# Kernel optimization log

Measured on AMD Instinct MI355X. Metric: run time of the kernel, lower is better.

Reference implementation:

```python
import jax, jax.numpy as jnp
import numpy as np

HEADS = 4
HID = 32
IN_CH = 3
N = 50000
E = 800000


def setup_inputs() -> dict:
    key = jax.random.key(0)
    ks = jax.random.split(key, 16)
    d1 = HEADS * HID  # 128
    s = 0.1
    inp = {
        'x': jax.random.normal(ks[0], (N, IN_CH), jnp.float32),
        'edge_index': jax.random.randint(ks[1], (2, E), 0, N, jnp.int64),
        # layer 1: in=3 -> heads*hid
        'W1': jax.random.normal(ks[2], (IN_CH, d1), jnp.float32) * s,
        'as1': jax.random.normal(ks[3], (HEADS, HID), jnp.float32) * s,
        'ad1': jax.random.normal(ks[4], (HEADS, HID), jnp.float32) * s,
        'b1': jnp.zeros((d1,), jnp.float32),
        # layer 2: 128 -> 128
        'W2': jax.random.normal(ks[5], (d1, d1), jnp.float32) * s,
        'as2': jax.random.normal(ks[6], (HEADS, HID), jnp.float32) * s,
        'ad2': jax.random.normal(ks[7], (HEADS, HID), jnp.float32) * s,
        'b2': jnp.zeros((d1,), jnp.float32),
        # layer 3: 128 -> 128
        'W3': jax.random.normal(ks[8], (d1, d1), jnp.float32) * s,
        'as3': jax.random.normal(ks[9], (HEADS, HID), jnp.float32) * s,
        'ad3': jax.random.normal(ks[10], (HEADS, HID), jnp.float32) * s,
        'b3': jnp.zeros((d1,), jnp.float32),
        # classifier: 128 -> 1
        'cW': jax.random.normal(ks[11], (d1, 1), jnp.float32) * s,
        'cb': jnp.zeros((1,), jnp.float32),
    }
    return inp


def _gat_layer(x, src, dst, n, W, a_s, a_d, b):
    """PyG GATConv (concat=True, negative_slope=0.2, self-loops already added)."""
    xp = (x @ W).reshape(n, HEADS, HID)              # [N,H,C]
    al_s = jnp.einsum('nhc,hc->nh', xp, a_s)          # [N,H]
    al_d = jnp.einsum('nhc,hc->nh', xp, a_d)          # [N,H]
    e = jax.nn.leaky_relu(al_s[src] + al_d[dst], 0.2)  # [E',H]
    emax = jax.ops.segment_max(e, dst, num_segments=n)  # segment softmax over dst
    ex = jnp.exp(e - emax[dst])
    den = jax.ops.segment_sum(ex, dst, num_segments=n)
    alpha = ex / (den[dst] + 1e-16)                   # [E',H]
    msg = xp[src] * alpha[:, :, None]                 # [E',H,C]
    out = jax.ops.segment_sum(msg, dst, num_segments=n)  # [N,H,C]
    return out.reshape(n, HEADS * HID) + b


def reference(x, edge_index, W1, as1, ad1, b1, W2, as2, ad2, b2, W3, as3, ad3, b3, cW, cb):
    n = x.shape[0]
    loops = jnp.arange(n, dtype=edge_index.dtype)
    src = jnp.concatenate([edge_index[0], loops])     # add self-loops (PyG default)
    dst = jnp.concatenate([edge_index[1], loops])
    h = jax.nn.elu(_gat_layer(x, src, dst, n, W1, as1, ad1, b1))
    h = jax.nn.elu(_gat_layer(h, src, dst, n, W2, as2, ad2, b2))
    h = jax.nn.elu(_gat_layer(h, src, dst, n, W3, as3, ad3, b3))
    logits = (h @ cW + cb)[:, 0]                      # [N]
    return jax.nn.sigmoid(logits)                     # eval mode output
```

## Files before the change

kernel.cpp:

```cpp
#include <hip/hip_runtime.h>
#include <math.h>

typedef unsigned int uint_t;
typedef __attribute__((ext_vector_type(8))) short bf16x8;
typedef __attribute__((ext_vector_type(4))) float f32x4;

#define BK_SHIFT 7
#define BK_NODES 128
#define MAXBK 512
#define PART_CHUNK 4096
#define SORT_CAP 4096

__device__ __forceinline__ float lrelu(float x){ return x > 0.f ? x : 0.2f*x; }
__device__ __forceinline__ float sel4(float a, float b, float c, float d, int h){
    return h==0 ? a : (h==1 ? b : (h==2 ? c : d));
}
__device__ __forceinline__ float wsum(float v){
    #pragma unroll
    for (int m = 1; m < 64; m <<= 1) v += __shfl_xor(v, m);
    return v;
}
__device__ __forceinline__ uint_t pack_bf2(float a, float b){
    uint_t ua = __float_as_uint(a); uint_t ub = __float_as_uint(b);
    ua += 0x7FFFu + ((ua >> 16) & 1u);
    ub += 0x7FFFu + ((ub >> 16) & 1u);
    return (ua >> 16) | (ub & 0xFFFF0000u);
}
__device__ __forceinline__ float bflo(uint_t u){ return __uint_as_float(u << 16); }
__device__ __forceinline__ float bfhi(uint_t u){ return __uint_as_float(u & 0xFFFF0000u); }
__device__ __forceinline__ bf16x8 mk_bf8(uint4 u){
    bf16x8 r;
    r[0]=(short)(u.x & 0xFFFFu); r[1]=(short)(u.x >> 16);
    r[2]=(short)(u.y & 0xFFFFu); r[3]=(short)(u.y >> 16);
    r[4]=(short)(u.z & 0xFFFFu); r[5]=(short)(u.z >> 16);
    r[6]=(short)(u.w & 0xFFFFu); r[7]=(short)(u.w >> 16);
    return r;
}


__global__ __launch_bounds__(256) void bucket_count(const int* __restrict__ ei, int E, int N,
                                                    int* __restrict__ bkcnt){
    __shared__ int h[MAXBK];
    int t = threadIdx.x;
    for (int i = t; i < MAXBK; i += 256) h[i] = 0;
    __syncthreads();
    int base = blockIdx.x * PART_CHUNK;
    int cnt = E + N - base; if (cnt > PART_CHUNK) cnt = PART_CHUNK; if (cnt < 0) cnt = 0;
    for (int i = t; i < cnt; i += 256){
        int idx = base + i;
        int d = (idx < E) ? ei[E + idx] : (idx - E);
        atomicAdd(&h[d >> BK_SHIFT], 1);
    }
    __syncthreads();
    for (int i = t; i < MAXBK; i += 256) if (h[i]) atomicAdd(&bkcnt[i], h[i]);
}

__global__ __launch_bounds__(512) void bucket_scan(const int* __restrict__ bkcnt,
                                                   int* __restrict__ bkoff,
                                                   int* __restrict__ gcursor,
                                                   int NBK, int EN){
    int t = threadIdx.x;
    __shared__ int sm[MAXBK];
    sm[t] = (t < NBK) ? bkcnt[t] : 0;
    __syncthreads();
    for (int off = 1; off < MAXBK; off <<= 1){
        int u = (t >= off) ? sm[t - off] : 0;
        __syncthreads();
        sm[t] += u;
        __syncthreads();
    }
    int excl = (t == 0) ? 0 : sm[t - 1];
    if (t < NBK){ bkoff[t] = excl; gcursor[t] = excl; }
    if (t == 0) bkoff[NBK] = EN;
}

__global__ __launch_bounds__(256) void partition_kernel(
        const int* __restrict__ ei, int E, int N,
        int* __restrict__ gcursor, uint_t* __restrict__ pairbuf, int NBK){
    __shared__ int hist[MAXBK];
    __shared__ int sA[MAXBK];
    __shared__ int destadj[MAXBK];
    __shared__ int cnt2[MAXBK];
    __shared__ uint_t staged[PART_CHUNK];
    __shared__ unsigned short sbk[PART_CHUNK];
    int t = threadIdx.x;
    int base = blockIdx.x * PART_CHUNK;
    int total = E + N;
    int cnt = total - base; if (cnt > PART_CHUNK) cnt = PART_CHUNK; if (cnt < 0) cnt = 0;

    for (int i = t; i < MAXBK; i += 256){ hist[i] = 0; cnt2[i] = 0; }
    __syncthreads();
    for (int i = t; i < cnt; i += 256){
        int idx = base + i;
        int d = (idx < E) ? ei[E + idx] : (idx - E);
        atomicAdd(&hist[d >> BK_SHIFT], 1);
    }
    __syncthreads();
    sA[t] = hist[t]; sA[t + 256] = hist[t + 256];
    __syncthreads();
    for (int off = 1; off < MAXBK; off <<= 1){
        int i0 = t, i1 = t + 256;
        int a0 = sA[i0] + ((i0 >= off) ? sA[i0 - off] : 0);
        int a1 = sA[i1] + ((i1 >= off) ? sA[i1 - off] : 0);
        __syncthreads();
        sA[i0] = a0; sA[i1] = a1;
        __syncthreads();
    }
    for (int b = t; b < NBK; b += 256){
        int c = hist[b];
        int gstart = (b == 0) ? 0 : sA[b - 1];
        int rbase = c > 0 ? atomicAdd(&gcursor[b], c) : 0;
        destadj[b] = rbase - gstart;
        cnt2[b] = gstart;
    }
    __syncthreads();
    for (int i = t; i < cnt; i += 256){
        int idx = base + i;
        int d, s;
        if (idx < E){ s = ei[idx]; d = ei[E + idx]; }
        else        { s = d = idx - E; }
        int b = d >> BK_SHIFT;
        int pos = atomicAdd(&cnt2[b], 1);
        staged[pos] = (uint_t)s | ((uint_t)(d & (BK_NODES - 1)) << 25);
        sbk[pos] = (unsigned short)b;
    }
    __syncthreads();
    for (int p = t; p < cnt; p += 256){
        int b = (int)sbk[p];
        pairbuf[destadj[b] + p] = staged[p];
    }
}

__global__ __launch_bounds__(256) void bucket_sort2(
        const uint_t* __restrict__ pairbuf, const int* __restrict__ bkoff,
        int* __restrict__ indptr, int* __restrict__ srcs, int N, int NBK, int EN){
    int b = blockIdx.x;
    int beg = bkoff[b], end = bkoff[b + 1];
    int cnt = end - beg;
    int nb = b << BK_SHIFT;
    __shared__ int nh[BK_NODES];
    __shared__ int noff[BK_NODES];
    __shared__ int outb[SORT_CAP];
    int t = threadIdx.x;
    if (t < BK_NODES) nh[t] = 0;
    __syncthreads();
    for (int i = t; i < cnt; i += 256){
        uint_t pr = pairbuf[beg + i];
        atomicAdd(&nh[(int)(pr >> 25)], 1);
    }
    __syncthreads();
    if (t < BK_NODES) noff[t] = nh[t];
    __syncthreads();
    for (int off = 1; off < BK_NODES; off <<= 1){
        int u = 0;
        if (t < BK_NODES && t >= off) u = noff[t - off];
        __syncthreads();
        if (t < BK_NODES) noff[t] += u;
        __syncthreads();
    }
    if (t < BK_NODES){
        int excl = noff[t] - nh[t];
        int node = nb + t;
        if (node < N) indptr[node] = beg + excl;
        nh[t] = excl;
    }
    if (b == NBK - 1 && t == 0) indptr[N] = EN;
    __syncthreads();
    if (cnt <= SORT_CAP){
        for (int i = t; i < cnt; i += 256){
            uint_t pr = pairbuf[beg + i];
            int pos = atomicAdd(&nh[(int)(pr >> 25)], 1);
            outb[pos] = (int)(pr & 0x1FFFFFFu);
        }
        __syncthreads();
        for (int i = t; i < cnt; i += 256) srcs[beg + i] = outb[i];
    } else {
        for (int i = t; i < cnt; i += 256){
            uint_t pr = pairbuf[beg + i];
            int pos = atomicAdd(&nh[(int)(pr >> 25)], 1);
            srcs[beg + pos] = (int)(pr & 0x1FFFFFFu);
        }
    }
}

__global__ __launch_bounds__(128) void linear_al(
        const float* __restrict__ in, const float* __restrict__ W,
        const float* __restrict__ as_, const float* __restrict__ ad_,
        uint_t* __restrict__ xp16, float* __restrict__ als, float* __restrict__ ald,
        int N, int K){
    __shared__ float hs[8 * 3];
    int t = threadIdx.x;
    int base = blockIdx.x * 8;
    int rows = N - base; if (rows > 8) rows = 8;
    for (int idx = t; idx < rows * K; idx += 128){
        int r = idx / K, k = idx - r * K;
        hs[r * K + k] = in[(size_t)(base + r) * K + k];
    }
    __syncthreads();
    float acc[8] = {0.f,0.f,0.f,0.f,0.f,0.f,0.f,0.f};
    for (int k = 0; k < K; ++k){
        float w = W[k * 128 + t];
        #pragma unroll
        for (int r = 0; r < 8; ++r) acc[r] += hs[r * K + k] * w;
    }
    float asv = as_[t], adv = ad_[t];
    for (int r = 0; r < rows; ++r){
        int row = base + r;
        float v = acc[r];
        float vo = __shfl_xor(v, 1);
        if (!(t & 1)) xp16[(size_t)row * 64 + (t >> 1)] = pack_bf2(v, vo);
        float vs = v * asv, vd = v * adv;
        #pragma unroll
        for (int m = 16; m >= 1; m >>= 1){
            vs += __shfl_xor(vs, m);
            vd += __shfl_xor(vd, m);
        }
        if ((t & 31) == 0){
            int h = t >> 5;
            als[row * 4 + h] = vs;
            ald[row * 4 + h] = vd;
        }
    }
}

__global__ __launch_bounds__(256) void wpack_kernel(
        const float* __restrict__ W2, const float* __restrict__ W3,
        uint_t* __restrict__ B2, uint_t* __restrict__ B3){
    int idx = blockIdx.x * 256 + threadIdx.x;
    const float* W = (idx < 8192) ? W2 : W3;
    uint_t* Bp = (idx < 8192) ? B2 : B3;
    int i = idx & 8191;
    int u = i & 3, c = (i >> 2) & 15, kg = (i >> 6) & 3, kb = (i >> 8) & 3, cb = (i >> 10) & 7;
    int k = kb * 32 + kg * 8 + 2 * u;
    int col = cb * 16 + c;
    Bp[i] = pack_bf2(W[k * 128 + col], W[(k + 1) * 128 + col]);
}

__global__ __launch_bounds__(256) void gemm_mfma(
        const uint_t* __restrict__ h16, const uint_t* __restrict__ bpack,
        const float* __restrict__ as_, const float* __restrict__ ad_,
        uint_t* __restrict__ xp16, float* __restrict__ als, float* __restrict__ ald,
        int N){
    int w = threadIdx.x >> 6;
    int l = threadIdx.x & 63;
    int stripe = blockIdx.x * 4 + w;
    int base = stripe * 16;
    if (base >= N) return;
    int r16 = l & 15;
    int kg  = l >> 4;
    int row = base + r16;
    int rowc = row < N ? row : N - 1;

    bf16x8 afr[4];
    const uint4* hrow = (const uint4*)(h16 + (size_t)rowc * 64);
    #pragma unroll
    for (int kb = 0; kb < 4; ++kb) afr[kb] = mk_bf8(hrow[kb * 4 + kg]);

    f32x4 acc[8];
    #pragma unroll
    for (int cb = 0; cb < 8; ++cb) acc[cb] = (f32x4){0.f, 0.f, 0.f, 0.f};

    const uint4* bp = (const uint4*)bpack;
    #pragma unroll
    for (int cb = 0; cb < 8; ++cb){
        #pragma unroll
        for (int kb = 0; kb < 4; ++kb){
            bf16x8 bfr = mk_bf8(bp[((cb * 4 + kb) * 4 + kg) * 16 + r16]);
            acc[cb] = __builtin_amdgcn_mfma_f32_16x16x32_bf16(afr[kb], bfr, acc[cb], 0, 0, 0);
        }
    }

    #pragma unroll
    for (int reg = 0; reg < 4; ++reg){
        int ro = base + kg * 4 + reg;
        bool wr = (ro < N) && ((r16 & 1) == 0);
        #pragma unroll
        for (int cb = 0; cb < 8; ++cb){
            float v  = acc[cb][reg];
            float vo = __shfl_xor(v, 1);
            if (wr) xp16[(size_t)ro * 64 + cb * 8 + (r16 >> 1)] = pack_bf2(v, vo);
        }
        #pragma unroll
        for (int h = 0; h < 4; ++h){
            float a0 = as_[h * 32 + r16],      a1 = as_[h * 32 + 16 + r16];
            float g0 = ad_[h * 32 + r16],      g1 = ad_[h * 32 + 16 + r16];
            float ps = acc[2 * h][reg] * a0 + acc[2 * h + 1][reg] * a1;
            float pd = acc[2 * h][reg] * g0 + acc[2 * h + 1][reg] * g1;
            ps += __shfl_xor(ps, 1); ps += __shfl_xor(ps, 2);
            ps += __shfl_xor(ps, 4); ps += __shfl_xor(ps, 8);
            pd += __shfl_xor(pd, 1); pd += __shfl_xor(pd, 2);
            pd += __shfl_xor(pd, 4); pd += __shfl_xor(pd, 8);
            if (r16 == 0 && ro < N){
                als[(size_t)ro * 4 + h] = ps;
                ald[(size_t)ro * 4 + h] = pd;
            }
        }
    }
}

__global__ __launch_bounds__(256, 8) void gat_agg4(
        const uint_t* __restrict__ xp16, const float4* __restrict__ als,
        const float4* __restrict__ ald,
        const int* __restrict__ indptr, const int* __restrict__ srcs,
        const float* __restrict__ bias,
        uint_t* __restrict__ hout, int N, int mode,
        const float* __restrict__ cW, const float* __restrict__ cb,
        float* __restrict__ fout){
    int wid = threadIdx.x >> 6;
    int l   = threadIdx.x & 63;
    int n = blockIdx.x * 4 + wid;
    __shared__ int   ssh[4][64];
    __shared__ float esh[4][64][4];
    if (n >= N) return;

    int beg = indptr[n], end = indptr[n + 1];
    float4 ad4 = ald[n];
    int h = l >> 4;

    float d0 = 0.f, d1 = 0.f, d2 = 0.f, d3 = 0.f;
    float ax = 0.f, ay = 0.f;

    for (int cbeg = beg; cbeg < end; cbeg += 64){
        int cnt = end - cbeg; if (cnt > 64) cnt = 64;
        if (l < cnt){
            int s = srcs[cbeg + l];
            ssh[wid][l] = s;
            float4 a4 = als[s];
            float p0 = __expf(lrelu(a4.x + ad4.x));
            float p1 = __expf(lrelu(a4.y + ad4.y));
            float p2 = __expf(lrelu(a4.z + ad4.z));
            float p3 = __expf(lrelu(a4.w + ad4.w));
            *((float4*)&esh[wid][l][0]) = make_float4(p0, p1, p2, p3);
            d0 += p0; d1 += p1; d2 += p2; d3 += p3;
        }
        __builtin_amdgcn_wave_barrier();

        int j = 0;
        for (; j + 16 <= cnt; j += 16){
            int ss[16]; float ww[16]; uint_t uu[16];
            #pragma unroll
            for (int q = 0; q < 16; ++q){ ss[q] = ssh[wid][j+q]; ww[q] = esh[wid][j+q][h]; }
            #pragma unroll
            for (int q = 0; q < 16; ++q) uu[q] = xp16[(size_t)ss[q] * 64 + l];
            #pragma unroll
            for (int q = 0; q < 16; ++q){
                ax = fmaf(bflo(uu[q]), ww[q], ax);
                ay = fmaf(bfhi(uu[q]), ww[q], ay);
            }
        }
        for (; j + 8 <= cnt; j += 8){
            int ss[8]; float ww[8]; uint_t uu[8];
            #pragma unroll
            for (int q = 0; q < 8; ++q){ ss[q] = ssh[wid][j+q]; ww[q] = esh[wid][j+q][h]; }
            #pragma unroll
            for (int q = 0; q < 8; ++q) uu[q] = xp16[(size_t)ss[q] * 64 + l];
            #pragma unroll
            for (int q = 0; q < 8; ++q){
                ax = fmaf(bflo(uu[q]), ww[q], ax);
                ay = fmaf(bfhi(uu[q]), ww[q], ay);
            }
        }
        for (; j < cnt; ++j){
            int s = ssh[wid][j];
            float w = esh[wid][j][h];
            uint_t u = xp16[(size_t)s * 64 + l];
            ax = fmaf(bflo(u), w, ax);
            ay = fmaf(bfhi(u), w, ay);
        }
    }

    d0 = wsum(d0); d1 = wsum(d1); d2 = wsum(d2); d3 = wsum(d3);

    float dh = sel4(d0, d1, d2, d3, h);
    float inv = 1.f / (dh + 1e-16f);
    float2 b2 = ((const float2*)bias)[l];
    float vx = ax * inv + b2.x;
    float vy = ay * inv + b2.y;
    vx = vx > 0.f ? vx : (__expf(vx) - 1.f);
    vy = vy > 0.f ? vy : (__expf(vy) - 1.f);

    if (mode == 0){
        hout[(size_t)n * 64 + l] = pack_bf2(vx, vy);
    } else {
        float2 cw2 = ((const float2*)cW)[l];
        float p = vx * cw2.x + vy * cw2.y;
        p = wsum(p);
        if (l == 0){
            float logit = p + cb[0];
            fout[n] = 1.f / (1.f + __expf(-logit));
        }
    }
}

extern "C" void kernel_launch(void* const* d_in, const int* in_sizes, int n_in,
                              void* d_out, int out_size, void* d_ws, size_t ws_size,
                              hipStream_t stream){
    const float* x   = (const float*)d_in[0];
    const int*   ei  = (const int*)d_in[1];
    const float* W1  = (const float*)d_in[2];
    const float* as1 = (const float*)d_in[3];
    const float* ad1 = (const float*)d_in[4];
    const float* b1  = (const float*)d_in[5];
    const float* W2  = (const float*)d_in[6];
    const float* as2 = (const float*)d_in[7];
    const float* ad2 = (const float*)d_in[8];
    const float* b2  = (const float*)d_in[9];
    const float* W3  = (const float*)d_in[10];
    const float* as3 = (const float*)d_in[11];
    const float* ad3 = (const float*)d_in[12];
    const float* b3  = (const float*)d_in[13];
    const float* cW  = (const float*)d_in[14];
    const float* cb  = (const float*)d_in[15];
    float* out = (float*)d_out;

    int N = in_sizes[0] / 3;
    int E = in_sizes[1] / 2;
    int EN = E + N;
    int NBK = (N + BK_NODES - 1) / BK_NODES;

    char* ws = (char*)d_ws;
    size_t off = 0;
    auto alloc = [&](size_t bytes) -> void* {
        void* p = ws + off;
        off += (bytes + 255) & ~(size_t)255;
        return p;
    };
    int*    indptr  = (int*)alloc((size_t)(N + 1) * 4);
    int*    srcs    = (int*)alloc((size_t)EN * 4);
    uint_t* pairbuf = (uint_t*)alloc((size_t)EN * 4);
    uint_t* XP      = (uint_t*)alloc((size_t)N * 64 * 4);
    uint_t* H16     = (uint_t*)alloc((size_t)N * 64 * 4);
    float*  ALS     = (float*)alloc((size_t)N * 4 * 4);
    float*  ALD     = (float*)alloc((size_t)N * 4 * 4);
    int*    bkcnt   = (int*)alloc((size_t)MAXBK * 4);
    int*    bkoff   = (int*)alloc((size_t)(MAXBK + 1) * 4);
    int*    gcursor = (int*)alloc((size_t)MAXBK * 4);
    uint_t* BP2     = (uint_t*)alloc((size_t)8192 * 4);
    uint_t* BP3     = (uint_t*)alloc((size_t)8192 * 4);
    (void)ws_size;

    int pb = (EN + PART_CHUNK - 1) / PART_CHUNK;

    hipMemsetAsync(bkcnt, 0, (size_t)MAXBK * 4, stream);
    bucket_count<<<pb, 256, 0, stream>>>(ei, E, N, bkcnt);
    bucket_scan<<<1, 512, 0, stream>>>(bkcnt, bkoff, gcursor, NBK, EN);
    partition_kernel<<<pb, 256, 0, stream>>>(ei, E, N, gcursor, pairbuf, NBK);
    bucket_sort2<<<NBK, 256, 0, stream>>>(pairbuf, bkoff, indptr, srcs, N, NBK, EN);
    wpack_kernel<<<64, 256, 0, stream>>>(W2, W3, BP2, BP3);

    int ab = (N + 3) / 4;
    int gb = ((N + 15) / 16 + 3) / 4;
    linear_al<<<(N + 7) / 8, 128, 0, stream>>>(x, W1, as1, ad1, XP, ALS, ALD, N, 3);
    gat_agg4<<<ab, 256, 0, stream>>>(XP, (const float4*)ALS, (const float4*)ALD,
                                     indptr, srcs, b1, H16, N, 0, nullptr, nullptr, nullptr);
    gemm_mfma<<<gb, 256, 0, stream>>>(H16, BP2, as2, ad2, XP, ALS, ALD, N);
    gat_agg4<<<ab, 256, 0, stream>>>(XP, (const float4*)ALS, (const float4*)ALD,
                                     indptr, srcs, b2, H16, N, 0, nullptr, nullptr, nullptr);
    gemm_mfma<<<gb, 256, 0, stream>>>(H16, BP3, as3, ad3, XP, ALS, ALD, N);
    gat_agg4<<<ab, 256, 0, stream>>>(XP, (const float4*)ALS, (const float4*)ALD,
                                     indptr, srcs, b3, nullptr, N, 1, cW, cb, out);
}
```

Baseline: 227.3 us.

## Use fixed-size per-bucket slabs for CSR build and pack src/weight in LDS

Drops the separate bucket count and scan passes by giving each destination bucket a fixed SLAB-sized region, so partitioning atomically appends into slabs and the sort writes per-node begin/end arrays instead of a global indptr. The aggregation kernel takes indend and stores (weight, src) pairs per head in LDS so each lane does one 8-byte LDS read per edge. This saves two kernel launches and a full pass over the edge list. The risk is silent overflow if any bucket exceeds SLAB edges, since the large-bucket fallback path was removed, and the edge buffers grow to NBK*SLAB entries.

```diff
diff --git a/kernel.cpp b/kernel.cpp
--- a/kernel.cpp
+++ b/kernel.cpp
@@ -9,7 +9,7 @@
 #define BK_NODES 128
 #define MAXBK 512
 #define PART_CHUNK 4096
-#define SORT_CAP 4096
+#define SLAB 4096
 
 __device__ __forceinline__ float lrelu(float x){ return x > 0.f ? x : 0.2f*x; }
 __device__ __forceinline__ float sel4(float a, float b, float c, float d, int h){
@@ -38,43 +38,11 @@
 }
 
 
-__global__ __launch_bounds__(256) void bucket_count(const int* __restrict__ ei, int E, int N,
-                                                    int* __restrict__ bkcnt){
-    __shared__ int h[MAXBK];
-    int t = threadIdx.x;
-    for (int i = t; i < MAXBK; i += 256) h[i] = 0;
-    __syncthreads();
-    int base = blockIdx.x * PART_CHUNK;
-    int cnt = E + N - base; if (cnt > PART_CHUNK) cnt = PART_CHUNK; if (cnt < 0) cnt = 0;
-    for (int i = t; i < cnt; i += 256){
-        int idx = base + i;
-        int d = (idx < E) ? ei[E + idx] : (idx - E);
-        atomicAdd(&h[d >> BK_SHIFT], 1);
-    }
-    __syncthreads();
-    for (int i = t; i < MAXBK; i += 256) if (h[i]) atomicAdd(&bkcnt[i], h[i]);
-}
-
-__global__ __launch_bounds__(512) void bucket_scan(const int* __restrict__ bkcnt,
-                                                   int* __restrict__ bkoff,
-                                                   int* __restrict__ gcursor,
-                                                   int NBK, int EN){
-    int t = threadIdx.x;
-    __shared__ int sm[MAXBK];
-    sm[t] = (t < NBK) ? bkcnt[t] : 0;
-    __syncthreads();
-    for (int off = 1; off < MAXBK; off <<= 1){
-        int u = (t >= off) ? sm[t - off] : 0;
-        __syncthreads();
-        sm[t] += u;
-        __syncthreads();
-    }
-    int excl = (t == 0) ? 0 : sm[t - 1];
-    if (t < NBK){ bkoff[t] = excl; gcursor[t] = excl; }
-    if (t == 0) bkoff[NBK] = EN;
-}
-
-__global__ __launch_bounds__(256) void partition_kernel(
+__global__ void zero_kernel(int* __restrict__ gcursor){
+    gcursor[threadIdx.x] = 0;
+}
+
+__global__ __launch_bounds__(256) void partition_slab(
         const int* __restrict__ ei, int E, int N,
         int* __restrict__ gcursor, uint_t* __restrict__ pairbuf, int NBK){
     __shared__ int hist[MAXBK];
@@ -110,7 +78,7 @@
         int c = hist[b];
         int gstart = (b == 0) ? 0 : sA[b - 1];
         int rbase = c > 0 ? atomicAdd(&gcursor[b], c) : 0;
-        destadj[b] = rbase - gstart;
+        destadj[b] = b * SLAB + rbase - gstart;
         cnt2[b] = gstart;
     }
     __syncthreads();
@@ -131,21 +99,22 @@
     }
 }
 
-__global__ __launch_bounds__(256) void bucket_sort2(
-        const uint_t* __restrict__ pairbuf, const int* __restrict__ bkoff,
-        int* __restrict__ indptr, int* __restrict__ srcs, int N, int NBK, int EN){
+__global__ __launch_bounds__(256) void sort2_slab(
+        const uint_t* __restrict__ pairbuf, const int* __restrict__ gcursor,
+        int* __restrict__ indptr, int* __restrict__ indend,
+        int* __restrict__ srcs, int N, int NBK){
     int b = blockIdx.x;
-    int beg = bkoff[b], end = bkoff[b + 1];
-    int cnt = end - beg;
+    int cnt = gcursor[b];
+    int base = b * SLAB;
     int nb = b << BK_SHIFT;
     __shared__ int nh[BK_NODES];
     __shared__ int noff[BK_NODES];
-    __shared__ int outb[SORT_CAP];
+    __shared__ int outb[SLAB];
     int t = threadIdx.x;
     if (t < BK_NODES) nh[t] = 0;
     __syncthreads();
     for (int i = t; i < cnt; i += 256){
-        uint_t pr = pairbuf[beg + i];
+        uint_t pr = pairbuf[base + i];
         atomicAdd(&nh[(int)(pr >> 25)], 1);
     }
     __syncthreads();
@@ -159,28 +128,22 @@
         __syncthreads();
     }
     if (t < BK_NODES){
-        int excl = noff[t] - nh[t];
         int node = nb + t;
-        if (node < N) indptr[node] = beg + excl;
-        nh[t] = excl;
-    }
-    if (b == NBK - 1 && t == 0) indptr[N] = EN;
-    __syncthreads();
-    if (cnt <= SORT_CAP){
-        for (int i = t; i < cnt; i += 256){
-            uint_t pr = pairbuf[beg + i];
-            int pos = atomicAdd(&nh[(int)(pr >> 25)], 1);
-            outb[pos] = (int)(pr & 0x1FFFFFFu);
-        }
-        __syncthreads();
-        for (int i = t; i < cnt; i += 256) srcs[beg + i] = outb[i];
-    } else {
-        for (int i = t; i < cnt; i += 256){
-            uint_t pr = pairbuf[beg + i];
-            int pos = atomicAdd(&nh[(int)(pr >> 25)], 1);
-            srcs[beg + pos] = (int)(pr & 0x1FFFFFFu);
-        }
-    }
+        if (node < N){
+            int excl = noff[t] - nh[t];
+            indptr[node] = base + excl;
+            indend[node] = base + noff[t];
+        }
+        nh[t] = noff[t] - nh[t];
+    }
+    __syncthreads();
+    for (int i = t; i < cnt; i += 256){
+        uint_t pr = pairbuf[base + i];
+        int pos = atomicAdd(&nh[(int)(pr >> 25)], 1);
+        outb[pos] = (int)(pr & 0x1FFFFFFu);
+    }
+    __syncthreads();
+    for (int i = t; i < cnt; i += 256) srcs[base + i] = outb[i];
 }
 
 __global__ __launch_bounds__(128) void linear_al(
@@ -301,7 +264,8 @@
 __global__ __launch_bounds__(256, 8) void gat_agg4(
         const uint_t* __restrict__ xp16, const float4* __restrict__ als,
         const float4* __restrict__ ald,
-        const int* __restrict__ indptr, const int* __restrict__ srcs,
+        const int* __restrict__ indptr, const int* __restrict__ indend,
+        const int* __restrict__ srcs,
         const float* __restrict__ bias,
         uint_t* __restrict__ hout, int N, int mode,
         const float* __restrict__ cW, const float* __restrict__ cb,
@@ -309,11 +273,10 @@
     int wid = threadIdx.x >> 6;
     int l   = threadIdx.x & 63;
     int n = blockIdx.x * 4 + wid;
-    __shared__ int   ssh[4][64];
-    __shared__ float esh[4][64][4];
+    __shared__ uint2 swh[4][4][64];
     if (n >= N) return;
 
-    int beg = indptr[n], end = indptr[n + 1];
+    int beg = indptr[n], end = indend[n];
     float4 ad4 = ald[n];
     int h = l >> 4;
 
@@ -324,46 +287,50 @@
         int cnt = end - cbeg; if (cnt > 64) cnt = 64;
         if (l < cnt){
             int s = srcs[cbeg + l];
-            ssh[wid][l] = s;
             float4 a4 = als[s];
             float p0 = __expf(lrelu(a4.x + ad4.x));
             float p1 = __expf(lrelu(a4.y + ad4.y));
             float p2 = __expf(lrelu(a4.z + ad4.z));
             float p3 = __expf(lrelu(a4.w + ad4.w));
-            *((float4*)&esh[wid][l][0]) = make_float4(p0, p1, p2, p3);
+            swh[wid][0][l] = make_uint2(__float_as_uint(p0), (uint_t)s);
+            swh[wid][1][l] = make_uint2(__float_as_uint(p1), (uint_t)s);
+            swh[wid][2][l] = make_uint2(__float_as_uint(p2), (uint_t)s);
+            swh[wid][3][l] = make_uint2(__float_as_uint(p3), (uint_t)s);
             d0 += p0; d1 += p1; d2 += p2; d3 += p3;
         }
         __builtin_amdgcn_wave_barrier();
 
         int j = 0;
         for (; j + 16 <= cnt; j += 16){
-            int ss[16]; float ww[16]; uint_t uu[16];
-            #pragma unroll
-            for (int q = 0; q < 16; ++q){ ss[q] = ssh[wid][j+q]; ww[q] = esh[wid][j+q][h]; }
-            #pragma unroll
-            for (int q = 0; q < 16; ++q) uu[q] = xp16[(size_t)ss[q] * 64 + l];
+            uint2 sw[16]; uint_t uu[16];
+            #pragma unroll
+            for (int q = 0; q < 16; ++q) sw[q] = swh[wid][h][j+q];
+            #pragma unroll
+            for (int q = 0; q < 16; ++q) uu[q] = xp16[(size_t)sw[q].y * 64 + l];
             #pragma unroll
             for (int q = 0; q < 16; ++q){
-                ax = fmaf(bflo(uu[q]), ww[q], ax);
-                ay = fmaf(bfhi(uu[q]), ww[q], ay);
+                float w = __uint_as_float(sw[q].x);
+                ax = fmaf(bflo(uu[q]), w, ax);
+                ay = fmaf(bfhi(uu[q]), w, ay);
             }
         }
         for (; j + 8 <= cnt; j += 8){
-            int ss[8]; float ww[8]; uint_t uu[8];
-            #pragma unroll
-            for (int q = 0; q < 8; ++q){ ss[q] = ssh[wid][j+q]; ww[q] = esh[wid][j+q][h]; }
-            #pragma unroll
-            for (int q = 0; q < 8; ++q) uu[q] = xp16[(size_t)ss[q] * 64 + l];
+            uint2 sw[8]; uint_t uu[8];
+            #pragma unroll
+            for (int q = 0; q < 8; ++q) sw[q] = swh[wid][h][j+q];
+            #pragma unroll
+            for (int q = 0; q < 8; ++q) uu[q] = xp16[(size_t)sw[q].y * 64 + l];
             #pragma unroll
             for (int q = 0; q < 8; ++q){
-                ax = fmaf(bflo(uu[q]), ww[q], ax);
-                ay = fmaf(bfhi(uu[q]), ww[q], ay);
+                float w = __uint_as_float(sw[q].x);
+                ax = fmaf(bflo(uu[q]), w, ax);
+                ay = fmaf(bfhi(uu[q]), w, ay);
             }
         }
         for (; j < cnt; ++j){
-            int s = ssh[wid][j];
-            float w = esh[wid][j][h];
-            uint_t u = xp16[(size_t)s * 64 + l];
+            uint2 sw = swh[wid][h][j];
+            uint_t u = xp16[(size_t)sw.y * 64 + l];
+            float w = __uint_as_float(sw.x);
             ax = fmaf(bflo(u), w, ax);
             ay = fmaf(bfhi(u), w, ay);
         }
@@ -425,15 +392,14 @@
         off += (bytes + 255) & ~(size_t)255;
         return p;
     };
-    int*    indptr  = (int*)alloc((size_t)(N + 1) * 4);
-    int*    srcs    = (int*)alloc((size_t)EN * 4);
-    uint_t* pairbuf = (uint_t*)alloc((size_t)EN * 4);
+    int*    indptr  = (int*)alloc((size_t)N * 4);
+    int*    indend  = (int*)alloc((size_t)N * 4);
+    int*    srcs    = (int*)alloc((size_t)NBK * SLAB * 4);
+    uint_t* pairbuf = (uint_t*)alloc((size_t)NBK * SLAB * 4);
     uint_t* XP      = (uint_t*)alloc((size_t)N * 64 * 4);
     uint_t* H16     = (uint_t*)alloc((size_t)N * 64 * 4);
     float*  ALS     = (float*)alloc((size_t)N * 4 * 4);
     float*  ALD     = (float*)alloc((size_t)N * 4 * 4);
-    int*    bkcnt   = (int*)alloc((size_t)MAXBK * 4);
-    int*    bkoff   = (int*)alloc((size_t)(MAXBK + 1) * 4);
     int*    gcursor = (int*)alloc((size_t)MAXBK * 4);
     uint_t* BP2     = (uint_t*)alloc((size_t)8192 * 4);
     uint_t* BP3     = (uint_t*)alloc((size_t)8192 * 4);
@@ -441,22 +407,20 @@
 
     int pb = (EN + PART_CHUNK - 1) / PART_CHUNK;
 
-    hipMemsetAsync(bkcnt, 0, (size_t)MAXBK * 4, stream);
-    bucket_count<<<pb, 256, 0, stream>>>(ei, E, N, bkcnt);
-    bucket_scan<<<1, 512, 0, stream>>>(bkcnt, bkoff, gcursor, NBK, EN);
-    partition_kernel<<<pb, 256, 0, stream>>>(ei, E, N, gcursor, pairbuf, NBK);
-    bucket_sort2<<<NBK, 256, 0, stream>>>(pairbuf, bkoff, indptr, srcs, N, NBK, EN);
+    zero_kernel<<<1, MAXBK, 0, stream>>>(gcursor);
+    partition_slab<<<pb, 256, 0, stream>>>(ei, E, N, gcursor, pairbuf, NBK);
+    sort2_slab<<<NBK, 256, 0, stream>>>(pairbuf, gcursor, indptr, indend, srcs, N, NBK);
     wpack_kernel<<<64, 256, 0, stream>>>(W2, W3, BP2, BP3);
 
     int ab = (N + 3) / 4;
     int gb = ((N + 15) / 16 + 3) / 4;
     linear_al<<<(N + 7) / 8, 128, 0, stream>>>(x, W1, as1, ad1, XP, ALS, ALD, N, 3);
     gat_agg4<<<ab, 256, 0, stream>>>(XP, (const float4*)ALS, (const float4*)ALD,
-                                     indptr, srcs, b1, H16, N, 0, nullptr, nullptr, nullptr);
+                                     indptr, indend, srcs, b1, H16, N, 0, nullptr, nullptr, nullptr);
     gemm_mfma<<<gb, 256, 0, stream>>>(H16, BP2, as2, ad2, XP, ALS, ALD, N);
     gat_agg4<<<ab, 256, 0, stream>>>(XP, (const float4*)ALS, (const float4*)ALD,
-                                     indptr, srcs, b2, H16, N, 0, nullptr, nullptr, nullptr);
+                                     indptr, indend, srcs, b2, H16, N, 0, nullptr, nullptr, nullptr);
     gemm_mfma<<<gb, 256, 0, stream>>>(H16, BP3, as3, ad3, XP, ALS, ALD, N);
     gat_agg4<<<ab, 256, 0, stream>>>(XP, (const float4*)ALS, (const float4*)ALD,
-                                     indptr, srcs, b3, nullptr, N, 1, cW, cb, out);
-}
+                                     indptr, indend, srcs, b3, nullptr, N, 1, cW, cb, out);
+}
```

Measured after the change: 259.1 us. 14.0% more time.
